# Optimization experiments

Measured on AMD Instinct MI355X. Metric: run time of the kernel, lower is better.

The kernel has to match this reference:

```python
import jax, jax.numpy as jnp
import numpy as np

# Calibrated format: e4m3 (FpQuantizer(exp=4, man=3, mode='stpu')), fp max = 240
EXP = 4
MAN = 3
FP_MAX = 240.0
BIAS = 2 ** (EXP - 1) - 1  # 7
MIN_EXP = 1 - BIAS         # smallest normal exponent; below this -> subnormal LSB
TINY = 1e-38               # avoid log2(0)


def fp_fake_quantize(y):
    """Round y to nearest e4m3 value (with subnormals), clamp magnitude to FP_MAX.

    Matches float_quantize_stpu backend math: per-element exponent
    e = floor(log2|y|) clamped at the subnormal boundary, LSB = 2^(e - MAN),
    round-to-nearest on the mantissa grid, saturate at FP_MAX.
    """
    absy = jnp.abs(y)
    exp = jnp.floor(jnp.log2(jnp.maximum(absy, TINY)))
    exp = jnp.maximum(exp, float(MIN_EXP))
    lsb = jnp.exp2(exp - MAN)
    q = jnp.round(absy / lsb) * lsb
    q = jnp.minimum(q, FP_MAX)
    return jnp.sign(y) * q


def quantize_ste(y):
    # Straight-through estimator: value of fp_fake_quantize, gradient of identity
    return y + jax.lax.stop_gradient(fp_fake_quantize(y) - y)


def setup_inputs() -> dict:
    key = jax.random.key(0)
    k1, _ = jax.random.split(key)
    x = jax.random.normal(k1, (8, 4096, 4096), dtype=jnp.float32)
    # Calibrated scale = clamp(absmax, 1e-5, 1e20) / quantizer.max; use a fixed
    # representative value (absmax ~ 4.8 for N(0,1) at this size -> ~0.02)
    scale = jnp.full((1,), 0.02, dtype=jnp.float32)
    return {"x": x, "scale": scale}


def reference(x, scale):
    # inited forward: x_q = quantizer(x / scale) * scale
    s = scale.reshape(())  # scalar broadcast
    return quantize_ste(x / s) * s
```

## Files before the change

### kernel.cpp

```cpp
#include <hip/hip_runtime.h>
#include <stdint.h>


__global__ __launch_bounds__(256) void fq_e4m3_kernel(
    const float4* __restrict__ x4,
    const float* __restrict__ scale,
    float4* __restrict__ out4,
    int n4)
{
    int i = blockIdx.x * blockDim.x + threadIdx.x;
    if (i >= n4) return;

    const float s = scale[0];
    float4 v = x4[i];
    float r[4] = {v.x, v.y, v.z, v.w};

#pragma unroll
    for (int k = 0; k < 4; ++k) {
        float y = r[k] / s;
        uint32_t u  = __float_as_uint(y);
        uint32_t au = u & 0x7FFFFFFFu;
        uint32_t sg = u & 0x80000000u;

        uint32_t rn = au + (((au >> 20) & 1u) + 0x0007FFFFu);
        rn &= 0xFFF00000u;
        float qn = fminf(__uint_as_float(rn), 240.0f);

        float ay = __uint_as_float(au);
        float qs = (ay + 16384.0f) - 16384.0f;

        float q = (au < 0x3C800000u) ? qs : qn;

        q = __uint_as_float(__float_as_uint(q) | sg);
        r[k] = q * s;
    }

    out4[i] = make_float4(r[0], r[1], r[2], r[3]);
}

extern "C" void kernel_launch(void* const* d_in, const int* in_sizes, int n_in,
                              void* d_out, int out_size, void* d_ws, size_t ws_size,
                              hipStream_t stream) {
    const float* x     = (const float*)d_in[0];
    const float* scale = (const float*)d_in[1];
    float* out         = (float*)d_out;

    int n  = in_sizes[0];
    int n4 = n >> 2;
    int block = 256;
    int grid  = (n4 + block - 1) / block;

    fq_e4m3_kernel<<<grid, block, 0, stream>>>(
        (const float4*)x, scale, (float4*)out, n4);
}
```

Baseline: 805.6 us.

## Use grid-stride loop with 4x unroll and nontemporal loads/stores

Replaces the one-thread-per-float4 launch with a persistent grid capped at 2048 blocks, where each thread processes four float4 elements per iteration using nontemporal loads and stores. The aim is more memory-level parallelism and less cache pollution on a streaming workload. The per-element quantization math is unchanged, including the division. A capped grid risks underfilling the device if occupancy is limited.

```diff
diff --git a/kernel.cpp b/kernel.cpp
--- a/kernel.cpp
+++ b/kernel.cpp
@@ -2,40 +2,67 @@
 #include <stdint.h>
 
 
+typedef float f32x4 __attribute__((ext_vector_type(4)));
+
+__device__ __forceinline__ float fq1(float x, float s) {
+    float y = x / s;
+    uint32_t u  = __float_as_uint(y);
+    uint32_t au = u & 0x7FFFFFFFu;
+    uint32_t sg = u & 0x80000000u;
+
+    uint32_t rn = au + (((au >> 20) & 1u) + 0x0007FFFFu);
+    rn &= 0xFFF00000u;
+    float qn = fminf(__uint_as_float(rn), 240.0f);
+
+    float ay = __uint_as_float(au);
+    float qs = (ay + 16384.0f) - 16384.0f;
+
+    float q = (au < 0x3C800000u) ? qs : qn;
+
+    q = __uint_as_float(__float_as_uint(q) | sg);
+    return q * s;
+}
+
+__device__ __forceinline__ f32x4 fq4(f32x4 v, float s) {
+    f32x4 r;
+    r.x = fq1(v.x, s);
+    r.y = fq1(v.y, s);
+    r.z = fq1(v.z, s);
+    r.w = fq1(v.w, s);
+    return r;
+}
+
 __global__ __launch_bounds__(256) void fq_e4m3_kernel(
-    const float4* __restrict__ x4,
+    const f32x4* __restrict__ x4,
     const float* __restrict__ scale,
-    float4* __restrict__ out4,
+    f32x4* __restrict__ out4,
     int n4)
 {
+    const float s = scale[0];
+    const int stride = gridDim.x * blockDim.x;
     int i = blockIdx.x * blockDim.x + threadIdx.x;
-    if (i >= n4) return;
 
-    const float s = scale[0];
-    float4 v = x4[i];
-    float r[4] = {v.x, v.y, v.z, v.w};
+    for (; i + 3 * stride < n4; i += 4 * stride) {
+        f32x4 a = __builtin_nontemporal_load(&x4[i]);
+        f32x4 b = __builtin_nontemporal_load(&x4[i + stride]);
+        f32x4 c = __builtin_nontemporal_load(&x4[i + 2 * stride]);
+        f32x4 d = __builtin_nontemporal_load(&x4[i + 3 * stride]);
 
-#pragma unroll
-    for (int k = 0; k < 4; ++k) {
-        float y = r[k] / s;
-        uint32_t u  = __float_as_uint(y);
-        uint32_t au = u & 0x7FFFFFFFu;
-        uint32_t sg = u & 0x80000000u;
+        a = fq4(a, s);
+        b = fq4(b, s);
+        c = fq4(c, s);
+        d = fq4(d, s);
 
-        uint32_t rn = au + (((au >> 20) & 1u) + 0x0007FFFFu);
-        rn &= 0xFFF00000u;
-        float qn = fminf(__uint_as_float(rn), 240.0f);
-
-        float ay = __uint_as_float(au);
-        float qs = (ay + 16384.0f) - 16384.0f;
-
-        float q = (au < 0x3C800000u) ? qs : qn;
-
-        q = __uint_as_float(__float_as_uint(q) | sg);
-        r[k] = q * s;
+        __builtin_nontemporal_store(a, &out4[i]);
+        __builtin_nontemporal_store(b, &out4[i + stride]);
+        __builtin_nontemporal_store(c, &out4[i + 2 * stride]);
+        __builtin_nontemporal_store(d, &out4[i + 3 * stride]);
     }
-
-    out4[i] = make_float4(r[0], r[1], r[2], r[3]);
+    for (; i < n4; i += stride) {
+        f32x4 a = __builtin_nontemporal_load(&x4[i]);
+        a = fq4(a, s);
+        __builtin_nontemporal_store(a, &out4[i]);
+    }
 }
 
 extern "C" void kernel_launch(void* const* d_in, const int* in_sizes, int n_in,
@@ -47,9 +74,12 @@
 
     int n  = in_sizes[0];
     int n4 = n >> 2;
-    int block = 256;
-    int grid  = (n4 + block - 1) / block;
+
+    const int block = 256;
+    int grid = (n4 + block - 1) / block;
+    const int max_grid = 256 * 8;
+    if (grid > max_grid) grid = max_grid;
 
     fq_e4m3_kernel<<<grid, block, 0, stream>>>(
-        (const float4*)x, scale, (float4*)out, n4);
+        (const f32x4*)x, scale, (f32x4*)out, n4);
 }
```

New measurement: 874.3 us. +8.5%, slower.
